# Optimization experiments

Measured on AMD Instinct MI355X. Metric: run time of the kernel, lower is better.

## Reference

```python
import jax, jax.numpy as jnp
import numpy as np

B, L, D = 4, 1024, 1024
H, DK, DV = 16, 64, 64
TEMP = float(np.power(DK, 0.5))
LN_EPS = 1e-5


def setup_inputs() -> dict:
    key = jax.random.key(0)
    ks = jax.random.split(key, 11)
    s_qk = np.sqrt(2.0 / (D + DK))
    s_v = np.sqrt(2.0 / (D + DV))
    inp = {
        'q_in': jax.random.normal(ks[0], (B, L, D), jnp.float32),
        'k_in': jax.random.normal(ks[1], (B, L, D), jnp.float32),
        'v_in': jax.random.normal(ks[2], (B, L, D), jnp.float32),
        'Wq':  jax.random.normal(ks[3], (D, H * DK), jnp.float32) * s_qk,
        'Wq2': jax.random.normal(ks[4], (D, H * DK), jnp.float32) * s_qk,
        'Wk':  jax.random.normal(ks[5], (D, H * DK), jnp.float32) * s_qk,
        'Wv':  jax.random.normal(ks[6], (D, H * DV), jnp.float32) * s_v,
        'Wo':  jax.random.normal(ks[7], (H * DV, D), jnp.float32) * np.sqrt(2.0 / (H * DV + D)),
        'ln_g': jnp.ones((D,), jnp.float32),
        'ln_b': jnp.zeros((D,), jnp.float32),
        'Er':  jax.random.normal(ks[8], (H, L, DK), jnp.float32),
        # causal mask: True above the diagonal (positions to be masked with -inf)
        'mask': jnp.triu(jnp.ones((L, L), jnp.bool_), k=1)[None].repeat(B, axis=0),
    }
    return inp


def _skew(rel):
    # rel: [H, B, Lq, Lr] with Lr == Lq. Music-Transformer skew:
    # pad one zero column on the left, reshape, drop first row.
    h, b, lq, lr = rel.shape
    rel = jnp.pad(rel, ((0, 0), (0, 0), (0, 0), (1, 0)))        # [H,B,Lq,Lr+1]
    rel = rel.reshape(h, b, lr + 1, lq)                          # [H,B,Lr+1,Lq]
    return rel[:, :, 1:, :].reshape(h, b, lq, lr)                # [H,B,Lq,Lr]


def reference(q_in, k_in, v_in, Wq, Wq2, Wk, Wv, Wo, ln_g, ln_b, Er, mask):
    residual = q_in
    # projections -> [H, B, L, d]
    def proj(x, W, d):
        return x.reshape(B * L, D).dot(W).reshape(B, L, H, d).transpose(2, 0, 1, 3)
    q = proj(q_in, Wq, DK)
    q2 = proj(q_in, Wq2, DK)
    k = proj(k_in, Wk, DK)
    v = proj(v_in, Wv, DV)

    attn = jnp.einsum('hbqd,hbkd->hbqk', q, k) / TEMP            # [H,B,Lq,Lk]
    rel = _skew(jnp.einsum('hbqd,hrd->hbqr', q2, Er)) / TEMP     # [H,B,Lq,Lk]

    m = mask[None]                                               # [1,B,Lq,Lk]
    neg = jnp.float32(-jnp.inf)
    attn = jnp.where(m, neg, attn)
    rel = jnp.where(m, neg, rel)
    p = jax.nn.softmax(attn + rel, axis=-1)                      # [H,B,Lq,Lk]

    out = jnp.einsum('hbqk,hbkd->hbqd', p, v)                    # [H,B,Lq,DV]
    out = out.transpose(1, 2, 0, 3).reshape(B, L, H * DV)
    out = out.dot(Wo)                                            # dropout is identity (eval)

    x = out + residual
    mu = x.mean(-1, keepdims=True)
    var = x.var(-1, keepdims=True)
    y = (x - mu) * jax.lax.rsqrt(var + LN_EPS) * ln_g + ln_b
    return y, p
```

## Files before the change

kernel.cpp:

```cpp
#include <hip/hip_runtime.h>

typedef __bf16 bf16;
typedef __bf16 v8bf __attribute__((ext_vector_type(8)));
typedef float v4f __attribute__((ext_vector_type(4)));

#define B_ 4
#define L_ 1024
#define D_ 1024
#define NEG (-3.0e38f)
#define MFMA16(a, b, c) __builtin_amdgcn_mfma_f32_16x16x32_bf16(a, b, c, 0, 0, 0)

#define SWZ(base, r, cb) ((base) + ((r) * 128) + ((cb) ^ (((r) & 7) << 4)))

typedef const __attribute__((address_space(1))) void* gas_t;
typedef __attribute__((address_space(3))) void* las_t;
__device__ __forceinline__ void gl_lds16(const bf16* g, bf16* l)
{
    __builtin_amdgcn_global_load_lds((gas_t)g, (las_t)l, 16, 0, 0);
}

__global__ __launch_bounds__(256) void wconv_kernel(
    const float* __restrict__ w0, const float* __restrict__ w1,
    const float* __restrict__ w2, const float* __restrict__ w3,
    const float* __restrict__ w4, const float* __restrict__ er,
    const float* __restrict__ qin, const float* __restrict__ kin,
    const float* __restrict__ vin,
    bf16* __restrict__ wt, bf16* __restrict__ erb,
    bf16* __restrict__ qbf, bf16* __restrict__ kbf, bf16* __restrict__ vbf)
{
    int z = blockIdx.z;
    int tx = threadIdx.x, ty = threadIdx.y;
    if (z < 5) {
        const float* src = z == 0 ? w0 : z == 1 ? w1 : z == 2 ? w2 : z == 3 ? w3 : w4;
        bf16* dst = wt + (size_t)z * 1024 * 1024;
        __shared__ float t[32][33];
        int bx = blockIdx.x * 32, by = blockIdx.y * 32;
#pragma unroll
        for (int i = 0; i < 4; i++)
            t[ty + i * 8][tx] = src[(size_t)(by + ty + i * 8) * 1024 + bx + tx];
        __syncthreads();
#pragma unroll
        for (int i = 0; i < 4; i++)
            dst[(size_t)(bx + ty + i * 8) * 1024 + by + tx] = (bf16)t[tx][ty + i * 8];
    } else if (z == 5) {
        int base = (blockIdx.y * 32 + blockIdx.x) * 256 + ty * 32 + tx;
#pragma unroll
        for (int i = 0; i < 4; i++) {
            int idx = base + i * 262144;
            erb[idx] = (bf16)er[idx];
        }
    } else {
        const float* src = z == 6 ? qin : z == 7 ? kin : vin;
        bf16* dst = z == 6 ? qbf : z == 7 ? kbf : vbf;
        int id = (blockIdx.y * 32 + blockIdx.x) * 256 + ty * 32 + tx;
#pragma unroll
        for (int i = 0; i < 4; i++) {
            int j = id * 4 + i * 1048576;
            float4 v = *(const float4*)(src + j);
            union { bf16 h[4]; uint2 u; } t;
            t.h[0] = (bf16)v.x; t.h[1] = (bf16)v.y;
            t.h[2] = (bf16)v.z; t.h[3] = (bf16)v.w;
            *(uint2*)(dst + j) = t.u;
        }
    }
}

__global__ __launch_bounds__(256) void gemm128(
    const bf16* __restrict__ Ab, const bf16* __restrict__ Bt,
    float* __restrict__ Cf, bf16* __restrict__ Cb, bf16* __restrict__ Cb2,
    int K, int mode)
{
    __shared__ __align__(16) bf16 As[128 * 32];
    __shared__ __align__(16) bf16 Bs[128 * 32];
    int tid = threadIdx.x, lane = tid & 63, w = tid >> 6;
    int tn = blockIdx.x * 128, tm = blockIdx.y * 128;
    int wm = (w & 1) * 64, wn = (w >> 1) * 64;
    int m15 = lane & 15, rq = lane >> 4, kq = rq * 8;

    v4f acc[4][4];
#pragma unroll
    for (int m = 0; m < 4; ++m)
#pragma unroll
        for (int n = 0; n < 4; ++n)
#pragma unroll
            for (int i = 0; i < 4; ++i) acc[m][n][i] = 0.f;

    int sr = lane >> 2, scb = (lane & 3) * 8;
    const bf16* ga = Ab + (size_t)(tm + w * 32 + sr) * K + scb;
    const bf16* gb = Bt + (size_t)(tn + w * 32 + sr) * K + scb;
    bf16* la = As + w * 32 * 32;
    bf16* lb = Bs + w * 32 * 32;
    const size_t rowskip = (size_t)16 * K;

    for (int k0 = 0; k0 < K; k0 += 32) {
        gl_lds16(ga + k0, la);
        gl_lds16(ga + k0 + rowskip, la + 512);
        gl_lds16(gb + k0, lb);
        gl_lds16(gb + k0 + rowskip, lb + 512);
        __syncthreads();

        v8bf a[4], bfr[4];
#pragma unroll
        for (int m = 0; m < 4; ++m)
            a[m] = *(const v8bf*)&As[(wm + m * 16 + m15) * 32 + kq];
#pragma unroll
        for (int n = 0; n < 4; ++n)
            bfr[n] = *(const v8bf*)&Bs[(wn + n * 16 + m15) * 32 + kq];
#pragma unroll
        for (int m = 0; m < 4; ++m)
#pragma unroll
            for (int n = 0; n < 4; ++n)
                acc[m][n] = MFMA16(a[m], bfr[n], acc[m][n]);
        __syncthreads();
    }

#pragma unroll
    for (int m = 0; m < 4; ++m)
#pragma unroll
        for (int n = 0; n < 4; ++n)
#pragma unroll
            for (int i = 0; i < 4; ++i) {
                int row = tm + wm + m * 16 + rq * 4 + i;
                int col = tn + wn + n * 16 + m15;
                float v = acc[m][n][i];
                if (mode == 1)      Cf[(size_t)row * 1024 + col] = v;
                else if (mode == 0) {
                    bf16* dst = col < 1024 ? Cb : Cb2;
                    dst[(size_t)row * 1024 + (col & 1023)] = (bf16)v;
                } else {
                    int bb = row >> 10, l = row & 1023, hh = col >> 6, dv = col & 63;
                    Cb[(((size_t)(bb * 16 + hh) * 64 + dv) << 10) + l] = (bf16)v;
                }
            }
}

__global__ __launch_bounds__(256) void attn_mfma(
    const bf16* __restrict__ qb, const bf16* __restrict__ q2b,
    const bf16* __restrict__ kb, const bf16* __restrict__ vt,
    const bf16* __restrict__ erb, float* __restrict__ p_out,
    bf16* __restrict__ ab)
{
    int lin = blockIdx.x;
    int bh  = (lin & 7) | ((lin >> 7) << 3);
    int qt  = 15 - ((lin >> 3) & 15);
    int h = bh >> 2, b = bh & 3;
    int q0 = qt << 6;
    int tid = threadIdx.x, lane = tid & 63, w = tid >> 6;
    int m15 = lane & 15, rq = lane >> 4, kq = rq * 8;
    int li0 = w * 16 + rq * 4;

    __shared__ __align__(16) char KsB[8192];
    __shared__ __align__(16) char VtsB[8192];
    __shared__ __align__(16) char ErsB[2][8192];
    __shared__ __align__(16) float RELs[64][68];
    char* PsB = (char*)RELs;

    size_t pb = (size_t)(h * 4 + b) << 20;

    {
        int zr = tid >> 2, zc = (tid & 3) * 16;
        v4f zz = {0.f, 0.f, 0.f, 0.f};
        for (int kt = qt + 1; kt < 16; ++kt) {
            float* base = p_out + pb + ((size_t)(q0 + zr) << 10) + kt * 64 + zc;
#pragma unroll
            for (int i = 0; i < 4; ++i)
                __builtin_nontemporal_store(zz, (v4f*)(base + i * 4));
        }
    }

    for (int c = tid; c < 512; c += 256) {
        int r = c >> 3, col = (c & 7) * 8, cb = (c & 7) * 16;
        *(uint4*)SWZ(KsB, r, cb) =
            *(const uint4*)&qb[((size_t)((b << 10) + q0 + r) * 16 + h) * 64 + col];
        *(uint4*)SWZ(VtsB, r, cb) =
            *(const uint4*)&q2b[((size_t)((b << 10) + q0 + r) * 16 + h) * 64 + col];
    }
    __syncthreads();
    v8bf alo  = *(const v8bf*)SWZ(KsB,  w * 16 + m15, kq * 2);
    v8bf ahi  = *(const v8bf*)SWZ(KsB,  w * 16 + m15, kq * 2 + 64);
    v8bf a2lo = *(const v8bf*)SWZ(VtsB, w * 16 + m15, kq * 2);
    v8bf a2hi = *(const v8bf*)SWZ(VtsB, w * 16 + m15, kq * 2 + 64);

    float m_run[4], l_run[4], linv[4];
#pragma unroll
    for (int i = 0; i < 4; ++i) { m_run[i] = NEG; l_run[i] = 0.f; }
    v4f oacc[4];
#pragma unroll
    for (int t = 0; t < 4; ++t)
#pragma unroll
        for (int i = 0; i < 4; ++i) oacc[t][i] = 0.f;

    size_t kbase = ((size_t)(b << 10) * 16 + h) * 64;
    size_t vbase = ((size_t)(b * 16 + h) << 16);
    const bf16* erh = erb + ((size_t)h << 16);
    int nkt = qt + 1;

    for (int pass = 0; pass < 2; ++pass) {
        if (pass) {
#pragma unroll
            for (int i = 0; i < 4; ++i) linv[i] = 1.f / l_run[i];
        }
        for (int kt = 0; kt < nkt; ++kt) {
            int k0 = kt << 6;
            int rt0 = 15 - qt + kt;
            const bf16* erA = erh + (((size_t)rt0) << 12);
            __syncthreads();
            for (int c = tid; c < 512; c += 256) {
                int r = c >> 3, col = (c & 7) * 8, cb = (c & 7) * 16;
                *(uint4*)SWZ(KsB, r, cb) =
                    *(const uint4*)&kb[kbase + ((size_t)(k0 + r) << 10) + col];
                if (kt == 0)
                    *(uint4*)SWZ(ErsB[rt0 & 1], r, cb) =
                        *(const uint4*)&erA[((size_t)r << 6) + col];
                if (rt0 < 15)
                    *(uint4*)SWZ(ErsB[(rt0 + 1) & 1], r, cb) =
                        *(const uint4*)&erA[((size_t)(r + 64) << 6) + col];
                if (pass)
                    *(uint4*)SWZ(VtsB, r, cb) =
                        *(const uint4*)&vt[vbase + ((size_t)r << 10) + k0 + col];
            }
            __syncthreads();

            __builtin_amdgcn_s_setprio(1);
            {
                const char* EA = ErsB[rt0 & 1];
#pragma unroll
                for (int ct = 0; ct < 4; ++ct) {
                    v4f acc = {0.f, 0.f, 0.f, 0.f};
                    v8bf blo = *(const v8bf*)SWZ(EA, ct * 16 + m15, kq * 2);
                    v8bf bhi = *(const v8bf*)SWZ(EA, ct * 16 + m15, kq * 2 + 64);
                    acc = MFMA16(a2lo, blo, acc);
                    acc = MFMA16(a2hi, bhi, acc);
                    int c = ct * 16 + m15;
#pragma unroll
                    for (int i = 0; i < 4; ++i) {
                        int kl = c + li0 + i - 63;
                        if (kl >= 0) RELs[li0 + i][kl] = acc[i];
                    }
                }
            }
            if (rt0 < 15) {
                const char* EB = ErsB[(rt0 + 1) & 1];
#pragma unroll
                for (int ct = 0; ct < 4; ++ct) {
                    v4f acc = {0.f, 0.f, 0.f, 0.f};
                    v8bf blo = *(const v8bf*)SWZ(EB, ct * 16 + m15, kq * 2);
                    v8bf bhi = *(const v8bf*)SWZ(EB, ct * 16 + m15, kq * 2 + 64);
                    acc = MFMA16(a2lo, blo, acc);
                    acc = MFMA16(a2hi, bhi, acc);
                    int c = ct * 16 + m15;
#pragma unroll
                    for (int i = 0; i < 4; ++i) {
                        int kl = c + li0 + i + 1;
                        if (kl < 64) RELs[li0 + i][kl] = acc[i];
                    }
                }
            }
            v4f qk[4];
#pragma unroll
            for (int ct = 0; ct < 4; ++ct) {
                v4f acc = {0.f, 0.f, 0.f, 0.f};
                v8bf blo = *(const v8bf*)SWZ(KsB, ct * 16 + m15, kq * 2);
                v8bf bhi = *(const v8bf*)SWZ(KsB, ct * 16 + m15, kq * 2 + 64);
                acc = MFMA16(alo, blo, acc);
                qk[ct] = MFMA16(ahi, bhi, acc);
            }
            __builtin_amdgcn_s_setprio(0);

            float sc[4][4];
#pragma unroll
            for (int ct = 0; ct < 4; ++ct)
#pragma unroll
                for (int i = 0; i < 4; ++i) {
                    int li = li0 + i;
                    int j = ct * 16 + m15;
                    float v = (qk[ct][i] + RELs[li][j]) * 0.125f;
                    sc[ct][i] = (k0 + j > q0 + li) ? NEG : v;
                }
            if (!pass) {
#pragma unroll
                for (int i = 0; i < 4; ++i) {
                    float tmax = fmaxf(fmaxf(sc[0][i], sc[1][i]), fmaxf(sc[2][i], sc[3][i]));
#pragma unroll
                    for (int off = 1; off < 16; off <<= 1)
                        tmax = fmaxf(tmax, __shfl_xor(tmax, off));
                    float mn = fmaxf(m_run[i], tmax);
                    float es = __expf(sc[0][i] - mn) + __expf(sc[1][i] - mn)
                             + __expf(sc[2][i] - mn) + __expf(sc[3][i] - mn);
#pragma unroll
                    for (int off = 1; off < 16; off <<= 1)
                        es += __shfl_xor(es, off);
                    l_run[i] = l_run[i] * __expf(m_run[i] - mn) + es;
                    m_run[i] = mn;
                }
            } else {
                asm volatile("" ::: "memory");
#pragma unroll
                for (int ct = 0; ct < 4; ++ct)
#pragma unroll
                    for (int i = 0; i < 4; ++i) {
                        int li = li0 + i;
                        int j = ct * 16 + m15;
                        float p = __expf(sc[ct][i] - m_run[i]) * linv[i];
                        __builtin_nontemporal_store(
                            p, &p_out[pb + ((size_t)(q0 + li) << 10) + k0 + j]);
                        *(bf16*)(PsB + li * 272 + j * 2) = (bf16)p;
                    }
                asm volatile("" ::: "memory");
                v8bf plo = *(const v8bf*)(PsB + (w * 16 + m15) * 272 + kq * 2);
                v8bf phi = *(const v8bf*)(PsB + (w * 16 + m15) * 272 + kq * 2 + 64);
                __builtin_amdgcn_s_setprio(1);
#pragma unroll
                for (int ct = 0; ct < 4; ++ct) {
                    v8bf blo = *(const v8bf*)SWZ(VtsB, ct * 16 + m15, kq * 2);
                    v8bf bhi = *(const v8bf*)SWZ(VtsB, ct * 16 + m15, kq * 2 + 64);
                    oacc[ct] = MFMA16(plo, blo, oacc[ct]);
                    oacc[ct] = MFMA16(phi, bhi, oacc[ct]);
                }
                __builtin_amdgcn_s_setprio(0);
            }
        }
    }

#pragma unroll
    for (int ct = 0; ct < 4; ++ct)
#pragma unroll
        for (int i = 0; i < 4; ++i)
            ab[((size_t)((b << 10) + q0 + li0 + i) * 16 + h) * 64 + ct * 16 + m15] =
                (bf16)oacc[ct][i];
}

__global__ __launch_bounds__(256) void ln_kernel(
    const float* __restrict__ y0, const float* __restrict__ res,
    const float* __restrict__ g, const float* __restrict__ bb,
    float* __restrict__ y)
{
    int row = blockIdx.x, tid = threadIdx.x, lane = tid & 63, w = tid >> 6;
    __shared__ float rs[4], rq2[4];
    const float* xr = y0 + (size_t)row * D_;
    const float* rr = res + (size_t)row * D_;
    float x[4], sum = 0.f, sq = 0.f;
#pragma unroll
    for (int i = 0; i < 4; i++) {
        int c = tid + i * 256;
        x[i] = xr[c] + rr[c];
        sum += x[i]; sq += x[i] * x[i];
    }
#pragma unroll
    for (int off = 32; off; off >>= 1) { sum += __shfl_xor(sum, off); sq += __shfl_xor(sq, off); }
    if (lane == 0) { rs[w] = sum; rq2[w] = sq; }
    __syncthreads();
    sum = rs[0] + rs[1] + rs[2] + rs[3];
    sq  = rq2[0] + rq2[1] + rq2[2] + rq2[3];
    float mean = sum * (1.f / D_);
    float var  = sq * (1.f / D_) - mean * mean;
    float inv  = rsqrtf(var + 1e-5f);
#pragma unroll
    for (int i = 0; i < 4; i++) {
        int c = tid + i * 256;
        y[(size_t)row * D_ + c] = (x[i] - mean) * inv * g[c] + bb[c];
    }
}

extern "C" void kernel_launch(void* const* d_in, const int* in_sizes, int n_in,
                              void* d_out, int out_size, void* d_ws, size_t ws_size,
                              hipStream_t stream)
{
    const float* q_in = (const float*)d_in[0];
    const float* k_in = (const float*)d_in[1];
    const float* v_in = (const float*)d_in[2];
    const float* Wq   = (const float*)d_in[3];
    const float* Wq2  = (const float*)d_in[4];
    const float* Wk   = (const float*)d_in[5];
    const float* Wv   = (const float*)d_in[6];
    const float* Wo   = (const float*)d_in[7];
    const float* ln_g = (const float*)d_in[8];
    const float* ln_b = (const float*)d_in[9];
    const float* Er   = (const float*)d_in[10];

    float* y_out = (float*)d_out;
    float* p_out = y_out + (size_t)B_ * L_ * D_;

    char* ws = (char*)d_ws;
    const size_t MB = 1024 * 1024;
    bf16*  wT  = (bf16*)(ws);
    bf16*  erb = (bf16*)(ws + 10 * MB);
    bf16*  qb  = (bf16*)(ws + 12 * MB);
    bf16*  q2b = (bf16*)(ws + 20 * MB);
    bf16*  kb  = (bf16*)(ws + 28 * MB);
    bf16*  vtb = (bf16*)(ws + 36 * MB);
    bf16*  ab  = (bf16*)(ws + 44 * MB);
    float* y0  = (float*)(ws + 52 * MB);

    bf16* qbf = (bf16*)((char*)p_out + 160 * MB);
    bf16* kbf = (bf16*)((char*)p_out + 168 * MB);
    bf16* vbf = (bf16*)((char*)p_out + 176 * MB);

    wconv_kernel<<<dim3(32, 32, 9), dim3(32, 8), 0, stream>>>(
        Wq, Wq2, Wk, Wv, Wo, Er, q_in, k_in, v_in, wT, erb, qbf, kbf, vbf);

    gemm128<<<dim3(16, 32), 256, 0, stream>>>(qbf, wT,          nullptr, qb,  q2b,     1024, 0);
    gemm128<<<dim3( 8, 32), 256, 0, stream>>>(kbf, wT + 2 * MB, nullptr, kb,  nullptr, 1024, 0);
    gemm128<<<dim3( 8, 32), 256, 0, stream>>>(vbf, wT + 3 * MB, nullptr, vtb, nullptr, 1024, 2);

    attn_mfma<<<dim3(1024), 256, 0, stream>>>(qb, q2b, kb, vtb, erb, p_out, ab);

    gemm128<<<dim3( 8, 32), 256, 0, stream>>>(ab, wT + 4 * MB, y0, nullptr, nullptr, 1024, 1);
    ln_kernel<<<4096, 256, 0, stream>>>(y0, q_in, ln_g, ln_b, y_out);
}
```

Baseline: 671.5 us.

## Double-buffer GEMM and attention loads, pair causal q-tiles per block

The projection GEMMs switch from 128x128 to 64x128 tiles, with double-buffered LDS staging so the next k-slice loads while the current one is multiplied, and the V-projection output is written with packed stores. The attention kernel pairs a long and a short causal query tile in each block to balance work, and prefetches K/V/Er tiles into registers while computing, using double/triple-buffered LDS. It also stages probabilities in LDS so the P output is written with coalesced vector stores, and adds launch_bounds(256,2). The cost is more LDS and registers and a more intricate buffer-index scheme.

```diff
diff --git a/kernel.cpp b/kernel.cpp
--- a/kernel.cpp
+++ b/kernel.cpp
@@ -3,6 +3,7 @@
 typedef __bf16 bf16;
 typedef __bf16 v8bf __attribute__((ext_vector_type(8)));
 typedef float v4f __attribute__((ext_vector_type(4)));
+typedef unsigned int v4u __attribute__((ext_vector_type(4)));
 
 #define B_ 4
 #define L_ 1024
@@ -10,7 +11,7 @@
 #define NEG (-3.0e38f)
 #define MFMA16(a, b, c) __builtin_amdgcn_mfma_f32_16x16x32_bf16(a, b, c, 0, 0, 0)
 
-#define SWZ(base, r, cb) ((base) + ((r) * 128) + ((cb) ^ (((r) & 7) << 4)))
+#define SWZ(base, r, cb) ((char*)(base) + ((r) * 128) + ((cb) ^ (((r) & 7) << 4)))
 
 typedef const __attribute__((address_space(1))) void* gas_t;
 typedef __attribute__((address_space(3))) void* las_t;
@@ -65,269 +66,329 @@
     }
 }
 
-__global__ __launch_bounds__(256) void gemm128(
+__global__ __launch_bounds__(256) void gemm64(
     const bf16* __restrict__ Ab, const bf16* __restrict__ Bt,
     float* __restrict__ Cf, bf16* __restrict__ Cb, bf16* __restrict__ Cb2,
     int K, int mode)
 {
-    __shared__ __align__(16) bf16 As[128 * 32];
-    __shared__ __align__(16) bf16 Bs[128 * 32];
+    __shared__ __align__(16) bf16 As[2][64 * 32];
+    __shared__ __align__(16) bf16 Bs[2][128 * 32];
     int tid = threadIdx.x, lane = tid & 63, w = tid >> 6;
-    int tn = blockIdx.x * 128, tm = blockIdx.y * 128;
-    int wm = (w & 1) * 64, wn = (w >> 1) * 64;
+    int tn = blockIdx.x * 128, tm = blockIdx.y * 64;
+    int wn = w * 32;
     int m15 = lane & 15, rq = lane >> 4, kq = rq * 8;
 
-    v4f acc[4][4];
+    v4f acc[4][2];
 #pragma unroll
     for (int m = 0; m < 4; ++m)
 #pragma unroll
-        for (int n = 0; n < 4; ++n)
+        for (int n = 0; n < 2; ++n)
 #pragma unroll
             for (int i = 0; i < 4; ++i) acc[m][n][i] = 0.f;
 
-    int sr = lane >> 2, scb = (lane & 3) * 8;
-    const bf16* ga = Ab + (size_t)(tm + w * 32 + sr) * K + scb;
-    const bf16* gb = Bt + (size_t)(tn + w * 32 + sr) * K + scb;
-    bf16* la = As + w * 32 * 32;
-    bf16* lb = Bs + w * 32 * 32;
-    const size_t rowskip = (size_t)16 * K;
-
+    int sr = lane >> 2, sc8 = (lane & 3) * 8;
+    const bf16* ga  = Ab + (size_t)(tm + w * 16 + sr) * K + sc8;
+    const bf16* gb0 = Bt + (size_t)(tn + w * 32 + sr) * K + sc8;
+    const bf16* gb1 = gb0 + (size_t)16 * K;
+
+#define GSTAGE(buf, k0s) { \
+    gl_lds16(ga  + (k0s), As[buf] + w * 16 * 32); \
+    gl_lds16(gb0 + (k0s), Bs[buf] + w * 32 * 32); \
+    gl_lds16(gb1 + (k0s), Bs[buf] + (w * 32 + 16) * 32); }
+
+    int cur = 0;
+    GSTAGE(0, 0);
+    __syncthreads();
     for (int k0 = 0; k0 < K; k0 += 32) {
-        gl_lds16(ga + k0, la);
-        gl_lds16(ga + k0 + rowskip, la + 512);
-        gl_lds16(gb + k0, lb);
-        gl_lds16(gb + k0 + rowskip, lb + 512);
+        if (k0 + 32 < K) GSTAGE(cur ^ 1, k0 + 32);
+        v8bf a[4], bb[2];
+#pragma unroll
+        for (int m = 0; m < 4; ++m)
+            a[m] = *(const v8bf*)&As[cur][(m * 16 + m15) * 32 + kq];
+#pragma unroll
+        for (int n = 0; n < 2; ++n)
+            bb[n] = *(const v8bf*)&Bs[cur][(wn + n * 16 + m15) * 32 + kq];
+#pragma unroll
+        for (int m = 0; m < 4; ++m)
+#pragma unroll
+            for (int n = 0; n < 2; ++n)
+                acc[m][n] = MFMA16(a[m], bb[n], acc[m][n]);
         __syncthreads();
-
-        v8bf a[4], bfr[4];
-#pragma unroll
-        for (int m = 0; m < 4; ++m)
-            a[m] = *(const v8bf*)&As[(wm + m * 16 + m15) * 32 + kq];
-#pragma unroll
-        for (int n = 0; n < 4; ++n)
-            bfr[n] = *(const v8bf*)&Bs[(wn + n * 16 + m15) * 32 + kq];
-#pragma unroll
-        for (int m = 0; m < 4; ++m)
-#pragma unroll
-            for (int n = 0; n < 4; ++n)
-                acc[m][n] = MFMA16(a[m], bfr[n], acc[m][n]);
-        __syncthreads();
+        cur ^= 1;
     }
+#undef GSTAGE
 
 #pragma unroll
     for (int m = 0; m < 4; ++m)
 #pragma unroll
-        for (int n = 0; n < 4; ++n)
-#pragma unroll
-            for (int i = 0; i < 4; ++i) {
-                int row = tm + wm + m * 16 + rq * 4 + i;
-                int col = tn + wn + n * 16 + m15;
-                float v = acc[m][n][i];
-                if (mode == 1)      Cf[(size_t)row * 1024 + col] = v;
-                else if (mode == 0) {
-                    bf16* dst = col < 1024 ? Cb : Cb2;
-                    dst[(size_t)row * 1024 + (col & 1023)] = (bf16)v;
-                } else {
-                    int bb = row >> 10, l = row & 1023, hh = col >> 6, dv = col & 63;
-                    Cb[(((size_t)(bb * 16 + hh) * 64 + dv) << 10) + l] = (bf16)v;
+        for (int n = 0; n < 2; ++n) {
+            int col = tn + wn + n * 16 + m15;
+            if (mode == 2) {
+                union { bf16 h[4]; uint2 u; } pk;
+#pragma unroll
+                for (int i = 0; i < 4; ++i) pk.h[i] = (bf16)acc[m][n][i];
+                int row0 = tm + m * 16 + rq * 4;
+                int bb2 = row0 >> 10, l = row0 & 1023, hh = col >> 6, dv = col & 63;
+                *(uint2*)&Cb[(((size_t)(bb2 * 16 + hh) * 64 + dv) << 10) + l] = pk.u;
+            } else {
+#pragma unroll
+                for (int i = 0; i < 4; ++i) {
+                    int row = tm + m * 16 + rq * 4 + i;
+                    float v = acc[m][n][i];
+                    if (mode == 1) Cf[(size_t)row * 1024 + col] = v;
+                    else {
+                        bf16* dst = col < 1024 ? Cb : Cb2;
+                        dst[(size_t)row * 1024 + (col & 1023)] = (bf16)v;
+                    }
                 }
             }
-}
-
-__global__ __launch_bounds__(256) void attn_mfma(
+        }
+}
+
+__global__ __launch_bounds__(256, 2) void attn_mfma(
     const bf16* __restrict__ qb, const bf16* __restrict__ q2b,
     const bf16* __restrict__ kb, const bf16* __restrict__ vt,
     const bf16* __restrict__ erb, float* __restrict__ p_out,
     bf16* __restrict__ ab)
 {
     int lin = blockIdx.x;
-    int bh  = (lin & 7) | ((lin >> 7) << 3);
-    int qt  = 15 - ((lin >> 3) & 15);
+    int bh  = (lin & 7) | ((lin >> 6) << 3);
+    int pp  = (lin >> 3) & 7;
     int h = bh >> 2, b = bh & 3;
-    int q0 = qt << 6;
     int tid = threadIdx.x, lane = tid & 63, w = tid >> 6;
     int m15 = lane & 15, rq = lane >> 4, kq = rq * 8;
     int li0 = w * 16 + rq * 4;
 
-    __shared__ __align__(16) char KsB[8192];
-    __shared__ __align__(16) char VtsB[8192];
-    __shared__ __align__(16) char ErsB[2][8192];
+    __shared__ __align__(16) char KsB[2][8192];
+    __shared__ __align__(16) char VtsB[2][8192];
+    __shared__ __align__(16) char ErsB[3][8192];
     __shared__ __align__(16) float RELs[64][68];
-    char* PsB = (char*)RELs;
+    char* RELsB = (char*)RELs;
 
     size_t pb = (size_t)(h * 4 + b) << 20;
-
-    {
-        int zr = tid >> 2, zc = (tid & 3) * 16;
-        v4f zz = {0.f, 0.f, 0.f, 0.f};
-        for (int kt = qt + 1; kt < 16; ++kt) {
-            float* base = p_out + pb + ((size_t)(q0 + zr) << 10) + kt * 64 + zc;
-#pragma unroll
-            for (int i = 0; i < 4; ++i)
-                __builtin_nontemporal_store(zz, (v4f*)(base + i * 4));
-        }
-    }
-
-    for (int c = tid; c < 512; c += 256) {
-        int r = c >> 3, col = (c & 7) * 8, cb = (c & 7) * 16;
-        *(uint4*)SWZ(KsB, r, cb) =
-            *(const uint4*)&qb[((size_t)((b << 10) + q0 + r) * 16 + h) * 64 + col];
-        *(uint4*)SWZ(VtsB, r, cb) =
-            *(const uint4*)&q2b[((size_t)((b << 10) + q0 + r) * 16 + h) * 64 + col];
-    }
-    __syncthreads();
-    v8bf alo  = *(const v8bf*)SWZ(KsB,  w * 16 + m15, kq * 2);
-    v8bf ahi  = *(const v8bf*)SWZ(KsB,  w * 16 + m15, kq * 2 + 64);
-    v8bf a2lo = *(const v8bf*)SWZ(VtsB, w * 16 + m15, kq * 2);
-    v8bf a2hi = *(const v8bf*)SWZ(VtsB, w * 16 + m15, kq * 2 + 64);
-
-    float m_run[4], l_run[4], linv[4];
-#pragma unroll
-    for (int i = 0; i < 4; ++i) { m_run[i] = NEG; l_run[i] = 0.f; }
-    v4f oacc[4];
-#pragma unroll
-    for (int t = 0; t < 4; ++t)
-#pragma unroll
-        for (int i = 0; i < 4; ++i) oacc[t][i] = 0.f;
-
     size_t kbase = ((size_t)(b << 10) * 16 + h) * 64;
     size_t vbase = ((size_t)(b * 16 + h) << 16);
     const bf16* erh = erb + ((size_t)h << 16);
-    int nkt = qt + 1;
-
-    for (int pass = 0; pass < 2; ++pass) {
-        if (pass) {
-#pragma unroll
-            for (int i = 0; i < 4; ++i) linv[i] = 1.f / l_run[i];
-        }
-        for (int kt = 0; kt < nkt; ++kt) {
-            int k0 = kt << 6;
-            int rt0 = 15 - qt + kt;
-            const bf16* erA = erh + (((size_t)rt0) << 12);
-            __syncthreads();
-            for (int c = tid; c < 512; c += 256) {
-                int r = c >> 3, col = (c & 7) * 8, cb = (c & 7) * 16;
-                *(uint4*)SWZ(KsB, r, cb) =
-                    *(const uint4*)&kb[kbase + ((size_t)(k0 + r) << 10) + col];
-                if (kt == 0)
-                    *(uint4*)SWZ(ErsB[rt0 & 1], r, cb) =
-                        *(const uint4*)&erA[((size_t)r << 6) + col];
-                if (rt0 < 15)
-                    *(uint4*)SWZ(ErsB[(rt0 + 1) & 1], r, cb) =
-                        *(const uint4*)&erA[((size_t)(r + 64) << 6) + col];
-                if (pass)
-                    *(uint4*)SWZ(VtsB, r, cb) =
-                        *(const uint4*)&vt[vbase + ((size_t)r << 10) + k0 + col];
+
+    int c0 = tid, c1 = tid + 256;
+    int r0s = c0 >> 3, col0 = (c0 & 7) * 8, cb0 = (c0 & 7) * 16;
+    int r1s = c1 >> 3, col1 = (c1 & 7) * 8, cb1 = (c1 & 7) * 16;
+
+#define LOADK(d0, d1, kt) { int kk = (kt) << 6; \
+    d0 = *(const uint4*)&kb[kbase + ((size_t)(kk + r0s) << 10) + col0]; \
+    d1 = *(const uint4*)&kb[kbase + ((size_t)(kk + r1s) << 10) + col1]; }
+#define LOADE(d0, d1, t) { const bf16* e = erh + ((size_t)(t) << 12); \
+    d0 = *(const uint4*)&e[(r0s << 6) + col0]; \
+    d1 = *(const uint4*)&e[(r1s << 6) + col1]; }
+#define LOADV(d0, d1, kt) { int kk = (kt) << 6; \
+    d0 = *(const uint4*)&vt[vbase + ((size_t)r0s << 10) + kk + col0]; \
+    d1 = *(const uint4*)&vt[vbase + ((size_t)r1s << 10) + kk + col1]; }
+#define STORE2(buf, v0, v1) { *(uint4*)SWZ(buf, r0s, cb0) = v0; \
+                              *(uint4*)SWZ(buf, r1s, cb1) = v1; }
+
+    for (int qs = 0; qs < 2; ++qs) {
+        int qt = qs ? pp : 15 - pp;
+        int q0 = qt << 6, nkt = qt + 1, t0 = 15 - qt;
+
+        {
+            int zr = tid >> 2, zc = (tid & 3) * 16;
+            v4f zz = {0.f, 0.f, 0.f, 0.f};
+            for (int kt = qt + 1; kt < 16; ++kt) {
+                float* basep = p_out + pb + ((size_t)(q0 + zr) << 10) + kt * 64 + zc;
+#pragma unroll
+                for (int i = 0; i < 4; ++i)
+                    __builtin_nontemporal_store(zz, (v4f*)(basep + i * 4));
+            }
+        }
+
+        {
+            uint4 a0 = *(const uint4*)&qb[((size_t)((b << 10) + q0 + r0s) * 16 + h) * 64 + col0];
+            uint4 a1 = *(const uint4*)&qb[((size_t)((b << 10) + q0 + r1s) * 16 + h) * 64 + col1];
+            uint4 b0 = *(const uint4*)&q2b[((size_t)((b << 10) + q0 + r0s) * 16 + h) * 64 + col0];
+            uint4 b1 = *(const uint4*)&q2b[((size_t)((b << 10) + q0 + r1s) * 16 + h) * 64 + col1];
+            STORE2(RELsB, a0, a1);
+            STORE2(RELsB + 8192, b0, b1);
+        }
+        __syncthreads();
+        v8bf alo  = *(const v8bf*)SWZ(RELsB,        w * 16 + m15, kq * 2);
+        v8bf ahi  = *(const v8bf*)SWZ(RELsB,        w * 16 + m15, kq * 2 + 64);
+        v8bf a2lo = *(const v8bf*)SWZ(RELsB + 8192, w * 16 + m15, kq * 2);
+        v8bf a2hi = *(const v8bf*)SWZ(RELsB + 8192, w * 16 + m15, kq * 2 + 64);
+
+        float m_run[4], l_run[4], linv[4];
+#pragma unroll
+        for (int i = 0; i < 4; ++i) { m_run[i] = NEG; l_run[i] = 0.f; }
+        v4f oacc[4];
+#pragma unroll
+        for (int t = 0; t < 4; ++t)
+#pragma unroll
+            for (int i = 0; i < 4; ++i) oacc[t][i] = 0.f;
+
+        for (int pass = 0; pass < 2; ++pass) {
+            if (pass) {
+#pragma unroll
+                for (int i = 0; i < 4; ++i) linv[i] = 1.f / l_run[i];
+            }
+            {
+                uint4 ka, kb2, e0a, e0b, e1a, e1b, va, vb2;
+                LOADK(ka, kb2, 0);
+                LOADE(e0a, e0b, t0);
+                bool hb = (t0 + 1) <= 15;
+                if (hb) LOADE(e1a, e1b, t0 + 1);
+                if (pass) LOADV(va, vb2, 0);
+                STORE2(KsB[0], ka, kb2);
+                STORE2(ErsB[t0 % 3], e0a, e0b);
+                if (hb) STORE2(ErsB[(t0 + 1) % 3], e1a, e1b);
+                if (pass) STORE2(VtsB[0], va, vb2);
             }
             __syncthreads();
 
-            __builtin_amdgcn_s_setprio(1);
-            {
-                const char* EA = ErsB[rt0 & 1];
+            uint4 nk0, nk1, ne0, ne1, nv0, nv1;
+            for (int kt = 0; kt < nkt; ++kt) {
+                int k0 = kt << 6;
+                int tA = t0 + kt;
+                bool hasB = tA < 15;
+                bool hasNext = (kt + 1) < nkt;
+                bool hasNE = hasNext && (tA + 2) <= 15;
+                if (hasNext) {
+                    LOADK(nk0, nk1, kt + 1);
+                    if (hasNE) LOADE(ne0, ne1, tA + 2);
+                    if (pass) LOADV(nv0, nv1, kt + 1);
+                }
+                char* Kb = KsB[kt & 1];
+                char* EA = ErsB[tA % 3];
+                char* EB = ErsB[(tA + 1) % 3];
+                char* Vb = VtsB[kt & 1];
+
+                __builtin_amdgcn_s_setprio(1);
 #pragma unroll
                 for (int ct = 0; ct < 4; ++ct) {
-                    v4f acc = {0.f, 0.f, 0.f, 0.f};
+                    v4f a4 = {0.f, 0.f, 0.f, 0.f};
                     v8bf blo = *(const v8bf*)SWZ(EA, ct * 16 + m15, kq * 2);
                     v8bf bhi = *(const v8bf*)SWZ(EA, ct * 16 + m15, kq * 2 + 64);
-                    acc = MFMA16(a2lo, blo, acc);
-                    acc = MFMA16(a2hi, bhi, acc);
+                    a4 = MFMA16(a2lo, blo, a4);
+                    a4 = MFMA16(a2hi, bhi, a4);
                     int c = ct * 16 + m15;
 #pragma unroll
                     for (int i = 0; i < 4; ++i) {
                         int kl = c + li0 + i - 63;
-                        if (kl >= 0) RELs[li0 + i][kl] = acc[i];
-                    }
-                }
-            }
-            if (rt0 < 15) {
-                const char* EB = ErsB[(rt0 + 1) & 1];
+                        if (kl >= 0) RELs[li0 + i][kl] = a4[i];
+                    }
+                }
+                if (hasB) {
+#pragma unroll
+                    for (int ct = 0; ct < 4; ++ct) {
+                        v4f a4 = {0.f, 0.f, 0.f, 0.f};
+                        v8bf blo = *(const v8bf*)SWZ(EB, ct * 16 + m15, kq * 2);
+                        v8bf bhi = *(const v8bf*)SWZ(EB, ct * 16 + m15, kq * 2 + 64);
+                        a4 = MFMA16(a2lo, blo, a4);
+                        a4 = MFMA16(a2hi, bhi, a4);
+                        int c = ct * 16 + m15;
+#pragma unroll
+                        for (int i = 0; i < 4; ++i) {
+                            int kl = c + li0 + i + 1;
+                            if (kl < 64) RELs[li0 + i][kl] = a4[i];
+                        }
+                    }
+                }
+                v4f qk[4];
 #pragma unroll
                 for (int ct = 0; ct < 4; ++ct) {
-                    v4f acc = {0.f, 0.f, 0.f, 0.f};
-                    v8bf blo = *(const v8bf*)SWZ(EB, ct * 16 + m15, kq * 2);
-                    v8bf bhi = *(const v8bf*)SWZ(EB, ct * 16 + m15, kq * 2 + 64);
-                    acc = MFMA16(a2lo, blo, acc);
-                    acc = MFMA16(a2hi, bhi, acc);
-                    int c = ct * 16 + m15;
-#pragma unroll
-                    for (int i = 0; i < 4; ++i) {
-                        int kl = c + li0 + i + 1;
-                        if (kl < 64) RELs[li0 + i][kl] = acc[i];
-                    }
-                }
-            }
-            v4f qk[4];
-#pragma unroll
-            for (int ct = 0; ct < 4; ++ct) {
-                v4f acc = {0.f, 0.f, 0.f, 0.f};
-                v8bf blo = *(const v8bf*)SWZ(KsB, ct * 16 + m15, kq * 2);
-                v8bf bhi = *(const v8bf*)SWZ(KsB, ct * 16 + m15, kq * 2 + 64);
-                acc = MFMA16(alo, blo, acc);
-                qk[ct] = MFMA16(ahi, bhi, acc);
-            }
-            __builtin_amdgcn_s_setprio(0);
-
-            float sc[4][4];
-#pragma unroll
-            for (int ct = 0; ct < 4; ++ct)
-#pragma unroll
-                for (int i = 0; i < 4; ++i) {
-                    int li = li0 + i;
-                    int j = ct * 16 + m15;
-                    float v = (qk[ct][i] + RELs[li][j]) * 0.125f;
-                    sc[ct][i] = (k0 + j > q0 + li) ? NEG : v;
-                }
-            if (!pass) {
-#pragma unroll
-                for (int i = 0; i < 4; ++i) {
-                    float tmax = fmaxf(fmaxf(sc[0][i], sc[1][i]), fmaxf(sc[2][i], sc[3][i]));
-#pragma unroll
-                    for (int off = 1; off < 16; off <<= 1)
-                        tmax = fmaxf(tmax, __shfl_xor(tmax, off));
-                    float mn = fmaxf(m_run[i], tmax);
-                    float es = __expf(sc[0][i] - mn) + __expf(sc[1][i] - mn)
-                             + __expf(sc[2][i] - mn) + __expf(sc[3][i] - mn);
-#pragma unroll
-                    for (int off = 1; off < 16; off <<= 1)
-                        es += __shfl_xor(es, off);
-                    l_run[i] = l_run[i] * __expf(m_run[i] - mn) + es;
-                    m_run[i] = mn;
-                }
-            } else {
-                asm volatile("" ::: "memory");
+                    v4f a4 = {0.f, 0.f, 0.f, 0.f};
+                    v8bf blo = *(const v8bf*)SWZ(Kb, ct * 16 + m15, kq * 2);
+                    v8bf bhi = *(const v8bf*)SWZ(Kb, ct * 16 + m15, kq * 2 + 64);
+                    a4 = MFMA16(alo, blo, a4);
+                    qk[ct] = MFMA16(ahi, bhi, a4);
+                }
+                __builtin_amdgcn_s_setprio(0);
+
+                float sc[4][4];
 #pragma unroll
                 for (int ct = 0; ct < 4; ++ct)
 #pragma unroll
                     for (int i = 0; i < 4; ++i) {
                         int li = li0 + i;
                         int j = ct * 16 + m15;
-                        float p = __expf(sc[ct][i] - m_run[i]) * linv[i];
-                        __builtin_nontemporal_store(
-                            p, &p_out[pb + ((size_t)(q0 + li) << 10) + k0 + j]);
-                        *(bf16*)(PsB + li * 272 + j * 2) = (bf16)p;
-                    }
-                asm volatile("" ::: "memory");
-                v8bf plo = *(const v8bf*)(PsB + (w * 16 + m15) * 272 + kq * 2);
-                v8bf phi = *(const v8bf*)(PsB + (w * 16 + m15) * 272 + kq * 2 + 64);
-                __builtin_amdgcn_s_setprio(1);
-#pragma unroll
-                for (int ct = 0; ct < 4; ++ct) {
-                    v8bf blo = *(const v8bf*)SWZ(VtsB, ct * 16 + m15, kq * 2);
-                    v8bf bhi = *(const v8bf*)SWZ(VtsB, ct * 16 + m15, kq * 2 + 64);
-                    oacc[ct] = MFMA16(plo, blo, oacc[ct]);
-                    oacc[ct] = MFMA16(phi, bhi, oacc[ct]);
-                }
-                __builtin_amdgcn_s_setprio(0);
+                        float v = (qk[ct][i] + RELs[li][j]) * 0.125f;
+                        if (!hasB) v = (j > li) ? NEG : v;
+                        sc[ct][i] = v;
+                    }
+                if (!pass) {
+#pragma unroll
+                    for (int i = 0; i < 4; ++i) {
+                        float tmax = fmaxf(fmaxf(sc[0][i], sc[1][i]), fmaxf(sc[2][i], sc[3][i]));
+#pragma unroll
+                        for (int off = 1; off < 16; off <<= 1)
+                            tmax = fmaxf(tmax, __shfl_xor(tmax, off));
+                        float mn = fmaxf(m_run[i], tmax);
+                        float es = __expf(sc[0][i] - mn) + __expf(sc[1][i] - mn)
+                                 + __expf(sc[2][i] - mn) + __expf(sc[3][i] - mn);
+#pragma unroll
+                        for (int off = 1; off < 16; off <<= 1)
+                            es += __shfl_xor(es, off);
+                        l_run[i] = l_run[i] * __expf(m_run[i] - mn) + es;
+                        m_run[i] = mn;
+                    }
+                } else {
+#pragma unroll
+                    for (int ct = 0; ct < 4; ++ct)
+#pragma unroll
+                        for (int i = 0; i < 4; ++i) {
+                            int li = li0 + i;
+                            int j = ct * 16 + m15;
+                            RELs[li][j] = __expf(sc[ct][i] - m_run[i]) * linv[i];
+                        }
+                    asm volatile("" ::: "memory");
+#pragma unroll
+                    for (int i2 = 0; i2 < 2; ++i2)
+#pragma unroll
+                        for (int jh = 0; jh < 2; ++jh) {
+                            int rr = w * 16 + (lane >> 3) + 8 * i2;
+                            v4u val = *(const v4u*)(RELsB + rr * 272 + (lane & 7) * 16 + 128 * jh);
+                            __builtin_nontemporal_store(val,
+                                (v4u*)(p_out + pb + ((size_t)(q0 + rr) << 10) + k0 + (lane & 7) * 4 + 32 * jh));
+                        }
+                    const float* pr = &RELs[w * 16 + m15][0];
+                    v4f f0 = *(const v4f*)(pr + kq);
+                    v4f f1 = *(const v4f*)(pr + kq + 4);
+                    v4f f2 = *(const v4f*)(pr + kq + 32);
+                    v4f f3 = *(const v4f*)(pr + kq + 36);
+                    v8bf plo, phi;
+#pragma unroll
+                    for (int j = 0; j < 4; ++j) {
+                        plo[j] = (bf16)f0[j]; plo[j + 4] = (bf16)f1[j];
+                        phi[j] = (bf16)f2[j]; phi[j + 4] = (bf16)f3[j];
+                    }
+                    __builtin_amdgcn_s_setprio(1);
+#pragma unroll
+                    for (int ct = 0; ct < 4; ++ct) {
+                        v8bf blo = *(const v8bf*)SWZ(Vb, ct * 16 + m15, kq * 2);
+                        v8bf bhi = *(const v8bf*)SWZ(Vb, ct * 16 + m15, kq * 2 + 64);
+                        oacc[ct] = MFMA16(plo, blo, oacc[ct]);
+                        oacc[ct] = MFMA16(phi, bhi, oacc[ct]);
+                    }
+                    __builtin_amdgcn_s_setprio(0);
+                }
+                if (hasNext) {
+                    STORE2(KsB[(kt + 1) & 1], nk0, nk1);
+                    if (hasNE) STORE2(ErsB[(tA + 2) % 3], ne0, ne1);
+                    if (pass) STORE2(VtsB[(kt + 1) & 1], nv0, nv1);
+                }
+                __syncthreads();
             }
         }
+
+#pragma unroll
+        for (int ct = 0; ct < 4; ++ct)
+#pragma unroll
+            for (int i = 0; i < 4; ++i)
+                ab[((size_t)((b << 10) + q0 + li0 + i) * 16 + h) * 64 + ct * 16 + m15] =
+                    (bf16)oacc[ct][i];
     }
-
-#pragma unroll
-    for (int ct = 0; ct < 4; ++ct)
-#pragma unroll
-        for (int i = 0; i < 4; ++i)
-            ab[((size_t)((b << 10) + q0 + li0 + i) * 16 + h) * 64 + ct * 16 + m15] =
-                (bf16)oacc[ct][i];
+#undef LOADK
+#undef LOADE
+#undef LOADV
+#undef STORE2
 }
 
 __global__ __launch_bounds__(256) void ln_kernel(
@@ -399,12 +460,12 @@
     wconv_kernel<<<dim3(32, 32, 9), dim3(32, 8), 0, stream>>>(
         Wq, Wq2, Wk, Wv, Wo, Er, q_in, k_in, v_in, wT, erb, qbf, kbf, vbf);
 
-    gemm128<<<dim3(16, 32), 256, 0, stream>>>(qbf, wT,          nullptr, qb,  q2b,     1024, 0);
-    gemm128<<<dim3( 8, 32), 256, 0, stream>>>(kbf, wT + 2 * MB, nullptr, kb,  nullptr, 1024, 0);
-    gemm128<<<dim3( 8, 32), 256, 0, stream>>>(vbf, wT + 3 * MB, nullptr, vtb, nullptr, 1024, 2);
-
-    attn_mfma<<<dim3(1024), 256, 0, stream>>>(qb, q2b, kb, vtb, erb, p_out, ab);
-
-    gemm128<<<dim3( 8, 32), 256, 0, stream>>>(ab, wT + 4 * MB, y0, nullptr, nullptr, 1024, 1);
+    gemm64<<<dim3(16, 64), 256, 0, stream>>>(qbf, wT,          nullptr, qb,  q2b,     1024, 0);
+    gemm64<<<dim3( 8, 64), 256, 0, stream>>>(kbf, wT + 2 * MB, nullptr, kb,  nullptr, 1024, 0);
+    gemm64<<<dim3( 8, 64), 256, 0, stream>>>(vbf, wT + 3 * MB, nullptr, vtb, nullptr, 1024, 2);
+
+    attn_mfma<<<dim3(512), 256, 0, stream>>>(qb, q2b, kb, vtb, erb, p_out, ab);
+
+    gemm64<<<dim3( 8, 64), 256, 0, stream>>>(ab, wT + 4 * MB, y0, nullptr, nullptr, 1024, 1);
     ln_kernel<<<4096, 256, 0, stream>>>(y0, q_in, ln_g, ln_b, y_out);
 }
```

After: 625.0 us. -6.9%, faster.
